# Kernel tuning notes

Measured on AMD Instinct MI355X. Metric: run time of the kernel, lower is better.

The kernel has to match this reference:

```python
import jax, jax.numpy as jnp
import numpy as np
from jax import lax

B, T, E, H, ENC, NUM_LAYERS = 256, 100, 300, 512, 1024, 3
FORGET_BIAS = 1.0  # BasicLSTMCell default


def lstm_scan(x, W, b):
    """BasicLSTMCell over time. x: [B,T,E], W: [E+H,4H], b: [4H] -> hs: [B,T,H]."""
    def step(carry, xt):
        c, h = carry
        z = jnp.concatenate([xt, h], axis=-1) @ W + b  # [B,4H]
        i, j, f, o = jnp.split(z, 4, axis=-1)  # TF gate order i, j, f, o
        c = c * jax.nn.sigmoid(f + FORGET_BIAS) + jax.nn.sigmoid(i) * jnp.tanh(j)
        h = jnp.tanh(c) * jax.nn.sigmoid(o)
        return (c, h), h
    init = (jnp.zeros((x.shape[0], W.shape[1] // 4), x.dtype),) * 2
    _, hs = lax.scan(step, init, jnp.swapaxes(x, 0, 1))  # scan over T
    return jnp.swapaxes(hs, 0, 1)  # [B,T,H]


def last_output(hs, lengths):
    # reverse_sequence + slice[:, 0, :] == output at step length-1
    return hs[jnp.arange(hs.shape[0]), lengths - 1]  # [B,H]


def setup_inputs() -> dict:
    key = jax.random.key(0)
    ks = jax.random.split(key, 10)
    scale = 0.01  # random_normal_initializer(stddev=1/100)
    return {
        "left_embed": jax.random.normal(ks[0], (B, T, E), jnp.float32),
        "left_lengths": jax.random.randint(ks[1], (B,), 1, T + 1, jnp.int32),
        "right_embed": jax.random.normal(ks[2], (B, T, E), jnp.float32),
        "right_lengths": jax.random.randint(ks[3], (B,), 1, T + 1, jnp.int32),
        "W_left": jax.random.normal(ks[4], (E + H, 4 * H), jnp.float32) / np.sqrt(E + H),
        "b_left": jnp.zeros((4 * H,), jnp.float32),
        "W_right": jax.random.normal(ks[5], (E + H, 4 * H), jnp.float32) / np.sqrt(E + H),
        "b_right": jnp.zeros((4 * H,), jnp.float32),
        "trans_weights": scale * jax.random.normal(ks[6], (2 * H, ENC), jnp.float32),
        "hidden_weights": scale * jax.random.normal(ks[7], (NUM_LAYERS - 1, ENC, ENC), jnp.float32),
    }


def reference(left_embed, left_lengths, right_embed, right_lengths,
              W_left, b_left, W_right, b_right, trans_weights, hidden_weights):
    l_last = last_output(lstm_scan(left_embed, W_left, b_left), left_lengths)
    r_last = last_output(lstm_scan(right_embed, W_right, b_right), right_lengths)
    ctx = jnp.concatenate([l_last, r_last], axis=1)  # [B, 2H]
    x = jax.nn.relu(ctx @ trans_weights)
    for i in range(hidden_weights.shape[0]):  # dropout keep_prob=1.0 -> identity
        x = jax.nn.relu(x @ hidden_weights[i])
    return x  # [B, ENC]
```

## Files before the change

kernel.cpp:

```cpp
#include <hip/hip_runtime.h>
#include <math.h>

#define EDIM 300
#define HDIM 512
#define TDIM 100
#define BDIM 256
#define KTOT 812
#define ENC  1024
#define NBLK 256

#define B_C     0u
#define B_HHI   1048576u
#define B_HLO   2097152u
#define B_WXF   3145728u
#define B_WHF   5767168u
#define B_CTX   9961472u
#define B_X1    11010048u
#define B_X2    12058624u
#define B_TWH   13107200u
#define B_TWL   19398656u
#define B_ZX    25690112u

typedef __attribute__((ext_vector_type(8))) short bf16x8;
typedef _Float16 f16x8 __attribute__((ext_vector_type(8)));
typedef __attribute__((ext_vector_type(8))) unsigned short u16x8;
typedef __attribute__((ext_vector_type(4))) float f32x4;

__device__ __forceinline__ float fast_sigmoid(float x) {
    return 1.0f / (1.0f + __expf(-x));
}
__device__ __forceinline__ float fast_tanh(float x) {
    float t = __expf(2.0f * x);
    return 1.0f - 2.0f / (t + 1.0f);
}
__device__ __forceinline__ unsigned short bf16_rne(float v) {
    unsigned int u = __float_as_uint(v);
    unsigned int r = (u + 0x7fffu + ((u >> 16) & 1u)) >> 16;
    return (unsigned short)r;
}
__device__ __forceinline__ float bf16_to_f(unsigned short h) {
    return __uint_as_float(((unsigned int)h) << 16);
}
__device__ __forceinline__ void split2(float v, unsigned short& hi, unsigned short& lo) {
    hi = bf16_rne(v);
    lo = bf16_rne(v - bf16_to_f(hi));
}
__device__ __forceinline__ unsigned short f16_bits(float v) {
    _Float16 h = (_Float16)v;
    return *(unsigned short*)&h;
}
__device__ __forceinline__ float f16_val(unsigned short u) {
    _Float16 h = *(_Float16*)&u;
    return (float)h;
}
__device__ __forceinline__ void split_f16(float v, unsigned short& hi, unsigned short& lo) {
    hi = f16_bits(v);
    lo = f16_bits(v - f16_val(hi));
}

__global__ void zero_kernel(float* __restrict__ p, int n) {
    int i = blockIdx.x * blockDim.x + threadIdx.x;
    if (i < n) p[i] = 0.0f;
}

__global__ __launch_bounds__(256) void prep_w_lstm(
    const float* __restrict__ WL, const float* __restrict__ WR, char* __restrict__ ws)
{
    __shared__ float tile[64 * 65];
    int bid = blockIdx.x;
    int d = bid / (13 * 32);
    int rem = bid - d * (13 * 32);
    int kt = rem >> 5;
    int ct = rem & 31;
    const int k0 = kt * 64;
    const float* W = d ? WR : WL;
    for (int pass = 0; pass < 16; ++pass) {
        int idx = pass * 256 + threadIdx.x;
        int kk = idx >> 6, c = idx & 63;
        int g = c >> 4, hl = c & 15;
        int col = g * HDIM + ct * 16 + hl;
        int kg = k0 + kk;
        tile[kk * 65 + c] = (kg < KTOT) ? W[(size_t)kg * 2048 + col] : 0.0f;
    }
    __syncthreads();
    unsigned short* wx = (unsigned short*)(ws + B_WXF) + (size_t)d * 2048 * 320;
    unsigned short* wh = (unsigned short*)(ws + B_WHF) + (size_t)d * 2048 * 512;
    for (int pass = 0; pass < 16; ++pass) {
        int idx = pass * 256 + threadIdx.x;
        int c = idx >> 6, kk = idx & 63;
        int kg = k0 + kk;
        unsigned short hv = f16_bits(tile[kk * 65 + c]);
        int cp = ct * 64 + c;
        if (kg < 320) wx[(size_t)cp * 320 + kg] = (kg < 300) ? hv : (unsigned short)0;
        if (kg >= 300 && kg < KTOT) wh[(size_t)cp * 512 + (kg - 300)] = hv;
    }
}

__global__ __launch_bounds__(256) void prep_w_tail(
    const float* __restrict__ TW, const float* __restrict__ HW, char* __restrict__ ws)
{
    __shared__ float tile[64 * 65];
    int bid = blockIdx.x;
    int l = bid / 256;
    int rem = bid - l * 256;
    int kt = rem >> 4, ct = rem & 15;
    const int k0 = kt * 64, n0 = ct * 64;
    const float* W = (l == 0) ? TW : (HW + (size_t)(l - 1) * ENC * ENC);
    for (int pass = 0; pass < 16; ++pass) {
        int idx = pass * 256 + threadIdx.x;
        int kk = idx >> 6, c = idx & 63;
        tile[kk * 65 + c] = W[(size_t)(k0 + kk) * ENC + n0 + c];
    }
    __syncthreads();
    unsigned short* wh = (unsigned short*)(ws + B_TWH) + (size_t)l * ENC * ENC;
    unsigned short* wl = (unsigned short*)(ws + B_TWL) + (size_t)l * ENC * ENC;
    for (int pass = 0; pass < 16; ++pass) {
        int idx = pass * 256 + threadIdx.x;
        int c = idx >> 6, kk = idx & 63;
        unsigned short hi, lo;
        split2(tile[kk * 65 + c], hi, lo);
        size_t o = (size_t)(n0 + c) * ENC + k0 + kk;
        wh[o] = hi;
        wl[o] = lo;
    }
}

__global__ __launch_bounds__(512, 1) void prep_zx(
    const float* __restrict__ xL, const float* __restrict__ xR,
    const float* __restrict__ bL, const float* __restrict__ bR,
    char* __restrict__ ws)
{
    __shared__ __align__(16) char smem[81920];
    const int ntile = blockIdx.x;
    const int m0    = blockIdx.y * 64;
    const int d     = blockIdx.z;
    const int n0    = ntile * 128;
    const float* __restrict__ x    = d ? xR : xL;
    const float* __restrict__ bias = d ? bR : bL;
    const unsigned short* __restrict__ Wxp = (const unsigned short*)(ws + B_WXF) + (size_t)d * 2048 * 320;
    unsigned short* __restrict__ zx = (unsigned short*)(ws + B_ZX) + (size_t)d * 25600 * 2048;

    const int tid = threadIdx.x;
    const int l   = tid & 63;
    const int w   = tid >> 6;
    const int kh  = w >> 2;
    const int ms  = w & 3;
    const int fr  = l & 15;
    const int fg  = l >> 4;

    #pragma unroll
    for (int j = 0; j < 10; ++j) {
        int c = j * 512 + tid;
        int frag = c >> 6, ls = c & 63;
        int khf = (frag >= 40) ? 1 : 0;
        int f2 = frag - khf * 40;
        int itf = f2 >> 3, nff = f2 & 7;
        int colp = n0 + nff * 16 + (ls & 15);
        int kk = khf * 160 + itf * 32 + (ls >> 4) * 8;
        *(uint4*)(smem + frag * 1024 + ls * 16) =
            *(const uint4*)(Wxp + (size_t)colp * 320 + kk);
    }
    __syncthreads();

    f32x4 acc[8] = {};
    const int rowX = m0 + ms * 16 + fr;
    const float* __restrict__ xrow = x + (size_t)rowX * EDIM;
    const int kb = kh * 160 + fg * 8;

    #pragma unroll
    for (int it = 0; it < 5; ++it) {
        const int kg = kb + it * 32;
        float4 f4a = (kg + 4 <= EDIM) ? *(const float4*)(xrow + kg) : make_float4(0.f, 0.f, 0.f, 0.f);
        float4 f4b = (kg + 8 <= EDIM) ? *(const float4*)(xrow + kg + 4) : make_float4(0.f, 0.f, 0.f, 0.f);
        u16x8 ahu, alu;
        float vv[8] = { f4a.x, f4a.y, f4a.z, f4a.w, f4b.x, f4b.y, f4b.z, f4b.w };
        #pragma unroll
        for (int i = 0; i < 8; ++i) {
            unsigned short hi, lo;
            split_f16(vv[i], hi, lo);
            ahu[i] = hi;
            alu[i] = lo;
        }
        const f16x8 ah = *(f16x8*)&ahu;
        const f16x8 al = *(f16x8*)&alu;
        #pragma unroll
        for (int nf = 0; nf < 8; ++nf) {
            const f16x8 bv = *(const f16x8*)(smem + ((kh * 40 + it * 8 + nf) << 10) + l * 16);
            acc[nf] = __builtin_amdgcn_mfma_f32_16x16x32_f16(ah, bv, acc[nf], 0, 0, 0);
            acc[nf] = __builtin_amdgcn_mfma_f32_16x16x32_f16(al, bv, acc[nf], 0, 0, 0);
        }
    }

    __syncthreads();
    float* red = (float*)smem;
    if (kh == 1) {
        #pragma unroll
        for (int nf = 0; nf < 8; ++nf)
            #pragma unroll
            for (int r = 0; r < 4; ++r)
                red[(ms * 16 + fg * 4 + r) * 132 + nf * 16 + fr] = acc[nf][r];
    }
    __syncthreads();
    if (kh == 0) {
        #pragma unroll
        for (int nf = 0; nf < 8; ++nf) {
            const int col = (nf & 3) * HDIM + (ntile * 2 + (nf >> 2)) * 16 + fr;
            const float bv = bias[col];
            #pragma unroll
            for (int r = 0; r < 4; ++r) {
                const int rm = m0 + ms * 16 + fg * 4 + r;
                float v = acc[nf][r] + red[(ms * 16 + fg * 4 + r) * 132 + nf * 16 + fr] + bv;
                zx[(size_t)rm * 2048 + n0 + nf * 16 + fr] = f16_bits(v);
            }
        }
    }
}

__global__ __launch_bounds__(512, 1) void lstm_step_h(
    const int* __restrict__ lenL, const int* __restrict__ lenR,
    char* __restrict__ ws, int t, int par)
{
    __shared__ __align__(16) char smem[65536];

    const int bid   = blockIdx.x;
    const int ntile = (bid & 7) * 4 + ((bid >> 3) & 3);
    const int mt    = bid >> 5;
    const int n0    = ntile * 64;
    const int d     = mt >> 2;
    const int brow  = (mt & 3) * 64;

    const int* __restrict__ len = d ? lenR : lenL;

    float* __restrict__ cbuf = (float*)(ws + B_C);
    const unsigned short* __restrict__ hh_prev = (const unsigned short*)(ws + B_HHI) + (size_t)par * 262144;
    const unsigned short* __restrict__ hl_prev = (const unsigned short*)(ws + B_HLO) + (size_t)par * 262144;
    unsigned short* __restrict__ hh_next = (unsigned short*)(ws + B_HHI) + (size_t)(par ^ 1) * 262144;
    unsigned short* __restrict__ hl_next = (unsigned short*)(ws + B_HLO) + (size_t)(par ^ 1) * 262144;
    const unsigned short* __restrict__ Whp = (const unsigned short*)(ws + B_WHF) + (size_t)d * 2048 * 512;
    const unsigned short* __restrict__ zx  = (const unsigned short*)(ws + B_ZX) + (size_t)d * 25600 * 2048;
    float* __restrict__ ctx = (float*)(ws + B_CTX);

    const int tid = threadIdx.x;
    const int l   = tid & 63;
    const int w   = tid >> 6;
    const int kh  = w >> 2;
    const int ms  = w & 3;
    const int fr  = l & 15;
    const int fg  = l >> 4;

    const int hcol = ntile * 16 + fr;
    const int row0 = brow + ms * 16 + fg * 4;
    const int4 len4 = *(const int4*)(len + row0);
    float c_arr[4];
    unsigned short zraw[16];
    if (kh == 0) {
        const size_t cb = (size_t)(d * BDIM + row0) * HDIM + hcol;
        c_arr[0] = cbuf[cb];
        c_arr[1] = cbuf[cb + HDIM];
        c_arr[2] = cbuf[cb + 2 * HDIM];
        c_arr[3] = cbuf[cb + 3 * HDIM];
        const size_t zb = ((size_t)row0 * TDIM + t) * 2048 + n0 + fr;
        #pragma unroll
        for (int r = 0; r < 4; ++r)
            #pragma unroll
            for (int nf = 0; nf < 4; ++nf)
                zraw[r * 4 + nf] = zx[zb + (size_t)r * (TDIM * 2048) + nf * 16];
    }

    {
        const unsigned short* __restrict__ Wsrc = Whp + (size_t)n0 * 512;
        #pragma unroll
        for (int j = 0; j < 8; ++j) {
            int c = j * 512 + tid;
            int frag = c >> 6, ls = c & 63;
            int colp = (frag & 3) * 16 + (ls & 15);
            int kk = (frag >> 5) * 256 + ((frag >> 2) & 7) * 32 + (ls >> 4) * 8;
            *(uint4*)(smem + frag * 1024 + ls * 16) =
                *(const uint4*)(Wsrc + (size_t)colp * 512 + kk);
        }
    }
    __syncthreads();

    f32x4 acc[4] = {};
    const size_t abase = (size_t)(d * BDIM + brow + ms * 16 + fr) * HDIM + kh * 256 + fg * 8;
    uint4 ahc = *(const uint4*)(hh_prev + abase);
    uint4 alc = *(const uint4*)(hl_prev + abase);
    #pragma unroll
    for (int it = 0; it < 8; ++it) {
        uint4 ahn, aln;
        if (it < 7) {
            ahn = *(const uint4*)(hh_prev + abase + (it + 1) * 32);
            aln = *(const uint4*)(hl_prev + abase + (it + 1) * 32);
        }
        const f16x8 ah = *(const f16x8*)&ahc;
        const f16x8 al = *(const f16x8*)&alc;
        #pragma unroll
        for (int nf = 0; nf < 4; ++nf) {
            const f16x8 bv = *(const f16x8*)(smem + ((kh * 32 + it * 4 + nf) << 10) + l * 16);
            acc[nf] = __builtin_amdgcn_mfma_f32_16x16x32_f16(ah, bv, acc[nf], 0, 0, 0);
            acc[nf] = __builtin_amdgcn_mfma_f32_16x16x32_f16(al, bv, acc[nf], 0, 0, 0);
        }
        if (it < 7) { ahc = ahn; alc = aln; }
    }

    __syncthreads();
    float* red = (float*)smem;
    if (kh == 1) {
        #pragma unroll
        for (int nf = 0; nf < 4; ++nf)
            #pragma unroll
            for (int r = 0; r < 4; ++r)
                red[(ms * 16 + fg * 4 + r) * 65 + nf * 16 + fr] = acc[nf][r];
    }
    __syncthreads();
    if (kh == 0) {
        const int lens[4] = { len4.x, len4.y, len4.z, len4.w };
        #pragma unroll
        for (int r = 0; r < 4; ++r) {
            const int row = row0 + r;
            const int rb = (ms * 16 + fg * 4 + r) * 65;
            const float iv = acc[0][r] + red[rb + 0 * 16 + fr] + f16_val(zraw[r * 4 + 0]);
            const float jv = acc[1][r] + red[rb + 1 * 16 + fr] + f16_val(zraw[r * 4 + 1]);
            const float fv = acc[2][r] + red[rb + 2 * 16 + fr] + f16_val(zraw[r * 4 + 2]);
            const float ov = acc[3][r] + red[rb + 3 * 16 + fr] + f16_val(zraw[r * 4 + 3]);
            const float c_new = c_arr[r] * fast_sigmoid(fv + 1.0f)
                              + fast_sigmoid(iv) * fast_tanh(jv);
            const float h_new = fast_tanh(c_new) * fast_sigmoid(ov);
            const size_t hidx = (size_t)(d * BDIM + row) * HDIM + hcol;
            cbuf[hidx] = c_new;
            unsigned short hh, hl2;
            split_f16(h_new, hh, hl2);
            hh_next[hidx] = hh;
            hl_next[hidx] = hl2;
            if (t == lens[r] - 1) {
                ctx[(size_t)row * (2 * HDIM) + d * HDIM + hcol] = h_new;
            }
        }
    }
}

#define TL_AS_HI(hf) ((hf) * 5120)
#define TL_AS_LO(hf) (10240 + (hf) * 5120)
#define TL_BS_HI(hf) (20480 + (hf) * 5120)
#define TL_BS_LO(hf) (30720 + (hf) * 5120)

__global__ __launch_bounds__(512, 2) void gemm_relu_mfma(
    const float* __restrict__ A, const unsigned short* __restrict__ Wh,
    const unsigned short* __restrict__ Wl, float* __restrict__ C)
{
    const int ntile = blockIdx.x & 15;
    const int mt    = blockIdx.x >> 4;
    const int n0    = ntile * 64;
    const int m0    = mt * 64;

    __shared__ __align__(16) char smem[40960];

    const int tid  = threadIdx.x;
    const int l    = tid & 63;
    const int w    = tid >> 6;
    const int kh   = w >> 2;
    const int ms   = w & 3;
    const int fr   = l & 15;
    const int fg   = l >> 4;
    const int arow = tid >> 3;
    const int q    = (tid & 7) * 4;

    f32x4 acc[4] = {};

    for (int it = 0; it < 16; ++it) {
        #pragma unroll
        for (int hf = 0; hf < 2; ++hf) {
            const int kg = hf * 512 + it * 32 + q;
            const float4 v = *(const float4*)(A + (size_t)(m0 + arow) * ENC + kg);
            ushort4 vh, vl;
            split2(v.x, vh.x, vl.x);
            split2(v.y, vh.y, vl.y);
            split2(v.z, vh.z, vl.z);
            split2(v.w, vh.w, vl.w);
            *(ushort4*)(smem + TL_AS_HI(hf) + (arow * 40 + q) * 2) = vh;
            *(ushort4*)(smem + TL_AS_LO(hf) + (arow * 40 + q) * 2) = vl;
            const size_t wo = (size_t)(n0 + arow) * ENC + kg;
            *(ushort4*)(smem + TL_BS_HI(hf) + (arow * 40 + q) * 2) = *(const ushort4*)(Wh + wo);
            *(ushort4*)(smem + TL_BS_LO(hf) + (arow * 40 + q) * 2) = *(const ushort4*)(Wl + wo);
        }
        __syncthreads();
        const int aoff = ((ms * 16 + fr) * 40 + fg * 8) * 2;
        const bf16x8 ah = *(const bf16x8*)(smem + TL_AS_HI(kh) + aoff);
        const bf16x8 al = *(const bf16x8*)(smem + TL_AS_LO(kh) + aoff);
        #pragma unroll
        for (int nf = 0; nf < 4; ++nf) {
            const int boff = ((nf * 16 + fr) * 40 + fg * 8) * 2;
            const bf16x8 bh = *(const bf16x8*)(smem + TL_BS_HI(kh) + boff);
            const bf16x8 bl = *(const bf16x8*)(smem + TL_BS_LO(kh) + boff);
            acc[nf] = __builtin_amdgcn_mfma_f32_16x16x32_bf16(ah, bh, acc[nf], 0, 0, 0);
            acc[nf] = __builtin_amdgcn_mfma_f32_16x16x32_bf16(ah, bl, acc[nf], 0, 0, 0);
            acc[nf] = __builtin_amdgcn_mfma_f32_16x16x32_bf16(al, bh, acc[nf], 0, 0, 0);
        }
        __syncthreads();
    }

    float* red = (float*)smem;
    if (kh == 1) {
        #pragma unroll
        for (int nf = 0; nf < 4; ++nf)
            #pragma unroll
            for (int r = 0; r < 4; ++r)
                red[(ms * 16 + fg * 4 + r) * 65 + nf * 16 + fr] = acc[nf][r];
    }
    __syncthreads();
    if (kh == 0) {
        #pragma unroll
        for (int nf = 0; nf < 4; ++nf) {
            #pragma unroll
            for (int r = 0; r < 4; ++r) {
                float v = acc[nf][r] + red[(ms * 16 + fg * 4 + r) * 65 + nf * 16 + fr];
                v = v > 0.f ? v : 0.f;
                const int row = m0 + ms * 16 + fg * 4 + r;
                C[(size_t)row * ENC + n0 + nf * 16 + fr] = v;
            }
        }
    }
}

extern "C" void kernel_launch(void* const* d_in, const int* in_sizes, int n_in,
                              void* d_out, int out_size, void* d_ws, size_t ws_size,
                              hipStream_t stream) {
    const float* xL   = (const float*)d_in[0];
    const int*   lenL = (const int*)  d_in[1];
    const float* xR   = (const float*)d_in[2];
    const int*   lenR = (const int*)  d_in[3];
    const float* WL   = (const float*)d_in[4];
    const float* bL   = (const float*)d_in[5];
    const float* WR   = (const float*)d_in[6];
    const float* bR   = (const float*)d_in[7];
    const float* TW   = (const float*)d_in[8];
    const float* HW   = (const float*)d_in[9];
    char* ws   = (char*)d_ws;
    float* out = (float*)d_out;

    zero_kernel<<<3072, 256, 0, stream>>>((float*)ws, 786432);
    prep_w_lstm<<<832, 256, 0, stream>>>(WL, WR, ws);
    prep_w_tail<<<768, 256, 0, stream>>>(TW, HW, ws);
    prep_zx<<<dim3(16, 400, 2), 512, 0, stream>>>(xL, xR, bL, bR, ws);

    for (int t = 0; t < TDIM; ++t) {
        lstm_step_h<<<NBLK, 512, 0, stream>>>(lenL, lenR, ws, t, t & 1);
    }

    float* ctx = (float*)(ws + B_CTX);
    float* x1  = (float*)(ws + B_X1);
    float* x2  = (float*)(ws + B_X2);
    const unsigned short* twh = (const unsigned short*)(ws + B_TWH);
    const unsigned short* twl = (const unsigned short*)(ws + B_TWL);
    gemm_relu_mfma<<<64, 512, 0, stream>>>(ctx, twh,                twl,                x1);
    gemm_relu_mfma<<<64, 512, 0, stream>>>(x1,  twh + 1024 * 1024, twl + 1024 * 1024,  x2);
    gemm_relu_mfma<<<64, 512, 0, stream>>>(x2,  twh + 2048 * 1024, twl + 2048 * 1024,  out);
}
```

Baseline: 1.425 ms.

## Pre-swizzle recurrent weights and store input projections time-major

Splits the LSTM weight prep into separate input and recurrent kernels. The recurrent weights are now written in the exact MFMA fragment order that each step block loads, so the per-step shared-memory fill becomes a contiguous copy with no index arithmetic. The precomputed input projection is staged through shared memory and written time-major ([t][b]), which makes the per-step gate loads contiguous across batch rows. The h prefetch is also deepened to two stages and moved ahead of the barrier, at the cost of a few extra registers.

```diff
diff --git a/kernel.cpp b/kernel.cpp
--- a/kernel.cpp
+++ b/kernel.cpp
@@ -5,7 +5,6 @@
 #define HDIM 512
 #define TDIM 100
 #define BDIM 256
-#define KTOT 812
 #define ENC  1024
 #define NBLK 256
 
@@ -23,7 +22,6 @@
 
 typedef __attribute__((ext_vector_type(8))) short bf16x8;
 typedef _Float16 f16x8 __attribute__((ext_vector_type(8)));
-typedef __attribute__((ext_vector_type(8))) unsigned short u16x8;
 typedef __attribute__((ext_vector_type(4))) float f32x4;
 
 __device__ __forceinline__ float fast_sigmoid(float x) {
@@ -63,13 +61,13 @@
     if (i < n) p[i] = 0.0f;
 }
 
-__global__ __launch_bounds__(256) void prep_w_lstm(
+__global__ __launch_bounds__(256) void prep_wx(
     const float* __restrict__ WL, const float* __restrict__ WR, char* __restrict__ ws)
 {
     __shared__ float tile[64 * 65];
     int bid = blockIdx.x;
-    int d = bid / (13 * 32);
-    int rem = bid - d * (13 * 32);
+    int d = bid / (5 * 32);
+    int rem = bid - d * (5 * 32);
     int kt = rem >> 5;
     int ct = rem & 31;
     const int k0 = kt * 64;
@@ -77,22 +75,51 @@
     for (int pass = 0; pass < 16; ++pass) {
         int idx = pass * 256 + threadIdx.x;
         int kk = idx >> 6, c = idx & 63;
-        int g = c >> 4, hl = c & 15;
+        int g = (c >> 4) & 3, hl = c & 15;
         int col = g * HDIM + ct * 16 + hl;
         int kg = k0 + kk;
-        tile[kk * 65 + c] = (kg < KTOT) ? W[(size_t)kg * 2048 + col] : 0.0f;
+        tile[kk * 65 + c] = (kg < EDIM) ? W[(size_t)kg * 2048 + col] : 0.0f;
     }
     __syncthreads();
     unsigned short* wx = (unsigned short*)(ws + B_WXF) + (size_t)d * 2048 * 320;
-    unsigned short* wh = (unsigned short*)(ws + B_WHF) + (size_t)d * 2048 * 512;
     for (int pass = 0; pass < 16; ++pass) {
         int idx = pass * 256 + threadIdx.x;
         int c = idx >> 6, kk = idx & 63;
-        int kg = k0 + kk;
-        unsigned short hv = f16_bits(tile[kk * 65 + c]);
-        int cp = ct * 64 + c;
-        if (kg < 320) wx[(size_t)cp * 320 + kg] = (kg < 300) ? hv : (unsigned short)0;
-        if (kg >= 300 && kg < KTOT) wh[(size_t)cp * 512 + (kg - 300)] = hv;
+        wx[(size_t)(ct * 64 + c) * 320 + k0 + kk] = f16_bits(tile[kk * 65 + c]);
+    }
+}
+
+__global__ __launch_bounds__(256) void prep_whf(
+    const float* __restrict__ WL, const float* __restrict__ WR, char* __restrict__ ws)
+{
+    __shared__ float tile[64 * 65];
+    int bid = blockIdx.x;
+    int d = bid >> 8;
+    int rem = bid & 255;
+    int kt = rem >> 5;
+    int ct = rem & 31;
+    const float* W = d ? WR : WL;
+    for (int pass = 0; pass < 16; ++pass) {
+        int idx = pass * 256 + threadIdx.x;
+        int kk = idx >> 6, c = idx & 63;
+        int g = (c >> 4) & 3, hl = c & 15;
+        int col = g * HDIM + ct * 16 + hl;
+        tile[kk * 65 + c] = W[(size_t)(300 + kt * 64 + kk) * 2048 + col];
+    }
+    __syncthreads();
+    unsigned short* dst = (unsigned short*)(ws + B_WHF) + ((size_t)(d * 32 + ct) * 64) * 512;
+    #pragma unroll
+    for (int p = 0; p < 2; ++p) {
+        int item = p * 256 + threadIdx.x;
+        int fl = item >> 6;
+        int ls = item & 63;
+        int itl = fl >> 2, nfl = fl & 3;
+        int frag = (kt >> 2) * 32 + ((kt & 3) * 2 + itl) * 4 + nfl;
+        __align__(16) unsigned short v[8];
+        #pragma unroll
+        for (int j = 0; j < 8; ++j)
+            v[j] = f16_bits(tile[(itl * 32 + (ls >> 4) * 8 + j) * 65 + nfl * 16 + (ls & 15)]);
+        *(uint4*)(dst + (size_t)frag * 512 + ls * 8) = *(uint4*)v;
     }
 }
 
@@ -138,7 +165,7 @@
     const float* __restrict__ x    = d ? xR : xL;
     const float* __restrict__ bias = d ? bR : bL;
     const unsigned short* __restrict__ Wxp = (const unsigned short*)(ws + B_WXF) + (size_t)d * 2048 * 320;
-    unsigned short* __restrict__ zx = (unsigned short*)(ws + B_ZX) + (size_t)d * 25600 * 2048;
+    unsigned short* __restrict__ zxd = (unsigned short*)(ws + B_ZX) + (size_t)d * TDIM * BDIM * 2048;
 
     const int tid = threadIdx.x;
     const int l   = tid & 63;
@@ -172,7 +199,7 @@
         const int kg = kb + it * 32;
         float4 f4a = (kg + 4 <= EDIM) ? *(const float4*)(xrow + kg) : make_float4(0.f, 0.f, 0.f, 0.f);
         float4 f4b = (kg + 8 <= EDIM) ? *(const float4*)(xrow + kg + 4) : make_float4(0.f, 0.f, 0.f, 0.f);
-        u16x8 ahu, alu;
+        __align__(16) unsigned short ahu[8], alu[8];
         float vv[8] = { f4a.x, f4a.y, f4a.z, f4a.w, f4b.x, f4b.y, f4b.z, f4b.w };
         #pragma unroll
         for (int i = 0; i < 8; ++i) {
@@ -181,8 +208,8 @@
             ahu[i] = hi;
             alu[i] = lo;
         }
-        const f16x8 ah = *(f16x8*)&ahu;
-        const f16x8 al = *(f16x8*)&alu;
+        const f16x8 ah = *(f16x8*)ahu;
+        const f16x8 al = *(f16x8*)alu;
         #pragma unroll
         for (int nf = 0; nf < 8; ++nf) {
             const f16x8 bv = *(const f16x8*)(smem + ((kh * 40 + it * 8 + nf) << 10) + l * 16);
@@ -193,6 +220,7 @@
 
     __syncthreads();
     float* red = (float*)smem;
+    unsigned short* outT = (unsigned short*)(smem + 49152);
     if (kh == 1) {
         #pragma unroll
         for (int nf = 0; nf < 8; ++nf)
@@ -208,11 +236,21 @@
             const float bv = bias[col];
             #pragma unroll
             for (int r = 0; r < 4; ++r) {
-                const int rm = m0 + ms * 16 + fg * 4 + r;
                 float v = acc[nf][r] + red[(ms * 16 + fg * 4 + r) * 132 + nf * 16 + fr] + bv;
-                zx[(size_t)rm * 2048 + n0 + nf * 16 + fr] = f16_bits(v);
+                outT[(ms * 16 + fg * 4 + r) * 128 + nf * 16 + fr] = f16_bits(v);
             }
         }
+    }
+    __syncthreads();
+    {
+        int row = tid >> 3, seg = tid & 7;
+        int rm = m0 + row;
+        int b = rm / 100;
+        int tt = rm - b * 100;
+        unsigned short* dstrow = zxd + ((size_t)(tt * 256 + b)) * 2048 + n0 + seg * 16;
+        const unsigned short* s = outT + row * 128 + seg * 16;
+        *(uint4*)(dstrow)     = *(const uint4*)(s);
+        *(uint4*)(dstrow + 8) = *(const uint4*)(s + 8);
     }
 }
 
@@ -236,8 +274,8 @@
     const unsigned short* __restrict__ hl_prev = (const unsigned short*)(ws + B_HLO) + (size_t)par * 262144;
     unsigned short* __restrict__ hh_next = (unsigned short*)(ws + B_HHI) + (size_t)(par ^ 1) * 262144;
     unsigned short* __restrict__ hl_next = (unsigned short*)(ws + B_HLO) + (size_t)(par ^ 1) * 262144;
-    const unsigned short* __restrict__ Whp = (const unsigned short*)(ws + B_WHF) + (size_t)d * 2048 * 512;
-    const unsigned short* __restrict__ zx  = (const unsigned short*)(ws + B_ZX) + (size_t)d * 25600 * 2048;
+    const unsigned short* __restrict__ WhF = (const unsigned short*)(ws + B_WHF);
+    const unsigned short* __restrict__ zxd = (const unsigned short*)(ws + B_ZX) + (size_t)d * TDIM * BDIM * 2048;
     float* __restrict__ ctx = (float*)(ws + B_CTX);
 
     const int tid = threadIdx.x;
@@ -259,48 +297,48 @@
         c_arr[1] = cbuf[cb + HDIM];
         c_arr[2] = cbuf[cb + 2 * HDIM];
         c_arr[3] = cbuf[cb + 3 * HDIM];
-        const size_t zb = ((size_t)row0 * TDIM + t) * 2048 + n0 + fr;
+        const unsigned short* zb = zxd + ((size_t)(t * 256 + row0)) * 2048 + n0 + fr;
         #pragma unroll
         for (int r = 0; r < 4; ++r)
             #pragma unroll
             for (int nf = 0; nf < 4; ++nf)
-                zraw[r * 4 + nf] = zx[zb + (size_t)r * (TDIM * 2048) + nf * 16];
+                zraw[r * 4 + nf] = zb[r * 2048 + nf * 16];
     }
 
     {
-        const unsigned short* __restrict__ Wsrc = Whp + (size_t)n0 * 512;
+        const unsigned short* __restrict__ wsrc = WhF + ((size_t)(d * 32 + ntile) * 64) * 512;
         #pragma unroll
         for (int j = 0; j < 8; ++j) {
-            int c = j * 512 + tid;
-            int frag = c >> 6, ls = c & 63;
-            int colp = (frag & 3) * 16 + (ls & 15);
-            int kk = (frag >> 5) * 256 + ((frag >> 2) & 7) * 32 + (ls >> 4) * 8;
-            *(uint4*)(smem + frag * 1024 + ls * 16) =
-                *(const uint4*)(Wsrc + (size_t)colp * 512 + kk);
-        }
-    }
+            int o = j * 512 + tid;
+            *(uint4*)(smem + o * 16) = *(const uint4*)(wsrc + (size_t)o * 8);
+        }
+    }
+
+    const size_t abase = (size_t)(d * BDIM + brow + ms * 16 + fr) * HDIM + kh * 256 + fg * 8;
+    uint4 pfh[2], pfl[2];
+    pfh[0] = *(const uint4*)(hh_prev + abase);
+    pfl[0] = *(const uint4*)(hl_prev + abase);
+    pfh[1] = *(const uint4*)(hh_prev + abase + 32);
+    pfl[1] = *(const uint4*)(hl_prev + abase + 32);
     __syncthreads();
 
     f32x4 acc[4] = {};
-    const size_t abase = (size_t)(d * BDIM + brow + ms * 16 + fr) * HDIM + kh * 256 + fg * 8;
-    uint4 ahc = *(const uint4*)(hh_prev + abase);
-    uint4 alc = *(const uint4*)(hl_prev + abase);
     #pragma unroll
     for (int it = 0; it < 8; ++it) {
-        uint4 ahn, aln;
-        if (it < 7) {
-            ahn = *(const uint4*)(hh_prev + abase + (it + 1) * 32);
-            aln = *(const uint4*)(hl_prev + abase + (it + 1) * 32);
-        }
-        const f16x8 ah = *(const f16x8*)&ahc;
-        const f16x8 al = *(const f16x8*)&alc;
+        const uint4 ch = pfh[it & 1];
+        const uint4 cl = pfl[it & 1];
+        if (it + 2 < 8) {
+            pfh[it & 1] = *(const uint4*)(hh_prev + abase + (it + 2) * 32);
+            pfl[it & 1] = *(const uint4*)(hl_prev + abase + (it + 2) * 32);
+        }
+        const f16x8 ah = *(const f16x8*)&ch;
+        const f16x8 al = *(const f16x8*)&cl;
         #pragma unroll
         for (int nf = 0; nf < 4; ++nf) {
             const f16x8 bv = *(const f16x8*)(smem + ((kh * 32 + it * 4 + nf) << 10) + l * 16);
             acc[nf] = __builtin_amdgcn_mfma_f32_16x16x32_f16(ah, bv, acc[nf], 0, 0, 0);
             acc[nf] = __builtin_amdgcn_mfma_f32_16x16x32_f16(al, bv, acc[nf], 0, 0, 0);
         }
-        if (it < 7) { ahc = ahn; alc = aln; }
     }
 
     __syncthreads();
@@ -439,7 +477,8 @@
     float* out = (float*)d_out;
 
     zero_kernel<<<3072, 256, 0, stream>>>((float*)ws, 786432);
-    prep_w_lstm<<<832, 256, 0, stream>>>(WL, WR, ws);
+    prep_wx<<<320, 256, 0, stream>>>(WL, WR, ws);
+    prep_whf<<<512, 256, 0, stream>>>(WL, WR, ws);
     prep_w_tail<<<768, 256, 0, stream>>>(TW, HW, ws);
     prep_zx<<<dim3(16, 400, 2), 512, 0, stream>>>(xL, xR, bL, bR, ws);
 
```

New measurement: 1.304 ms. -8.5%, faster.
